# Optimization experiments

Measured on AMD Instinct MI355X. Metric: run time of the kernel, lower is better.

The kernel has to match this reference:

```python
import jax, jax.numpy as jnp
import numpy as np

N, C, R = 8192, 512, 8
DK = C // R  # 64

def setup_inputs() -> dict:
    key = jax.random.key(0)
    k1, k2, kq, kk, kv = jax.random.split(key, 5)
    s = 0.05
    return {
        "im1": jax.random.normal(k1, (N, C), jnp.float32),
        "im2": jax.random.normal(k2, (N, C), jnp.float32),
        "Wq": jax.random.normal(kq, (C, DK), jnp.float32) * s,
        "Wk": jax.random.normal(kk, (C, DK), jnp.float32) * s,
        "Wv": jax.random.normal(kv, (C, C), jnp.float32) * s,
    }

def reference(im1, im2, Wq, Wk, Wv):
    # shared projections (weights stored as [in, out]; torch Linear is x @ W.T)
    im1_q = im1 @ Wq  # [N, DK]
    im1_k = im1 @ Wk  # [N, DK]
    im1_v = im1 @ Wv  # [N, C]
    im2_q = im2 @ Wq
    im2_k = im2 @ Wk
    im2_v = im2 @ Wv
    # cross attention (no scaling in original)
    im1_attn = jax.nn.softmax(im2_q @ im1_k.T, axis=-1)  # [N, N]
    im2_attn = jax.nn.softmax(im1_q @ im2_k.T, axis=-1)  # [N, N]
    im1_out = im1_attn @ im1_v + im1
    im2_out = im2_attn @ im2_v + im2
    return im1_out, im2_out
```

## Files before the change

### kernel.cpp

```cpp
#include <hip/hip_runtime.h>

#define NN 8192
#define CC 512
#define DKK 64

typedef float f32x4 __attribute__((ext_vector_type(4)));
typedef float f32x16 __attribute__((ext_vector_type(16)));
typedef _Float16 f16x8 __attribute__((ext_vector_type(8)));
typedef _Float16 f16x4 __attribute__((ext_vector_type(4)));

__device__ __forceinline__ f32x4 mfma16(f16x8 a, f16x8 b, f32x4 c) {
    return __builtin_amdgcn_mfma_f32_16x16x32_f16(a, b, c, 0, 0, 0);
}
__device__ __forceinline__ f32x16 mfma32(f16x8 a, f16x8 b, f32x16 c) {
    return __builtin_amdgcn_mfma_f32_32x32x16_f16(a, b, c, 0, 0, 0);
}
__device__ __forceinline__ f16x8 scl8(f16x8 v, float f) {
    _Float16 h = (_Float16)f;
    f16x8 r;
#pragma unroll
    for (int i = 0; i < 8; i++) r[i] = v[i] * h;
    return r;
}

__global__ void wtrans_all_kernel(const float* __restrict__ Wq, const float* __restrict__ Wk,
                                  const float* __restrict__ Wv,
                                  _Float16* __restrict__ Wqt, _Float16* __restrict__ Wkt,
                                  _Float16* __restrict__ Wvf) {
    int idx = blockIdx.x * 256 + threadIdx.x;
    if (idx < 32768) {
        int n = idx >> 9, k = idx & 511;
        Wqt[idx] = (_Float16)Wq[k * 64 + n];
    } else if (idx < 65536) {
        int j = idx - 32768;
        int n = j >> 9, k = j & 511;
        Wkt[j] = (_Float16)Wk[k * 64 + n];
    } else {
        int j = idx - 65536;
        int k16 = j & 15, c = (j >> 4) & 511, ks = j >> 13;
        Wvf[j] = (_Float16)Wv[(size_t)(16 * ks + k16) * 512 + c];
    }
}

__global__ __launch_bounds__(256) void proj_qk2_kernel(
    const float* __restrict__ im1, const float* __restrict__ im2,
    const _Float16* __restrict__ Wqt, const _Float16* __restrict__ Wkt,
    _Float16* __restrict__ Q1, _Float16* __restrict__ Kf1,
    _Float16* __restrict__ Q2, _Float16* __restrict__ Kf2)
{
    const float* X = blockIdx.y ? im2 : im1;
    _Float16* Q = blockIdx.y ? Q2 : Q1;
    _Float16* Kf = blockIdx.y ? Kf2 : Kf1;

    __shared__ __align__(16) _Float16 Wlds[128 * 512];

    const int tid = threadIdx.x;
    const int lane = tid & 63, wave = tid >> 6;
    const int n16 = lane & 15, quad = lane >> 4;

#pragma unroll
    for (int i = 0; i < 32; i++) {
        const int idx = tid + 256 * i;
        const int row = idx >> 6, ch = idx & 63;
        const _Float16* src = (row < 64) ? (Wqt + (size_t)row * 512 + ch * 8)
                                         : (Wkt + (size_t)(row - 64) * 512 + ch * 8);
        *(f16x8*)&Wlds[row * 512 + ((ch ^ (row & 7)) * 8)] = *(const f16x8*)src;
    }
    __syncthreads();

    const int arow = blockIdx.x * 64 + wave * 16 + n16;
    f32x4 acc[8];
#pragma unroll
    for (int i = 0; i < 8; i++) acc[i] = (f32x4){0.f, 0.f, 0.f, 0.f};

    const float* xbase = X + (size_t)arow * 512 + quad * 8;
    for (int kk = 0; kk < 16; kk++) {
        f32x4 xa = *(const f32x4*)(xbase + kk * 32);
        f32x4 xb = *(const f32x4*)(xbase + kk * 32 + 4);
        f16x8 afrag;
#pragma unroll
        for (int j = 0; j < 4; j++) { afrag[j] = (_Float16)xa[j]; afrag[4 + j] = (_Float16)xb[j]; }
#pragma unroll
        for (int t = 0; t < 8; t++) {
            const int row = t * 16 + n16;
            f16x8 bfr = *(const f16x8*)&Wlds[row * 512 + (((4 * kk + quad) ^ (row & 7)) * 8)];
            acc[t] = mfma16(afrag, bfr, acc[t]);
        }
    }
    const int rbase = blockIdx.x * 64 + wave * 16 + quad * 4;
#pragma unroll
    for (int t = 0; t < 4; t++)
#pragma unroll
        for (int r = 0; r < 4; r++) {
            Q[(size_t)(rbase + r) * 64 + t * 16 + n16] = (_Float16)acc[t][r];
            Kf[((size_t)(blockIdx.x * 4 + t) * 64 + (wave * 16 + quad * 4 + r)) * 16 + n16] =
                (_Float16)acc[4 + t][r];
        }
}

__global__ __launch_bounds__(256) void proj_vt_kernel(
    const float* __restrict__ im1, const float* __restrict__ im2,
    const _Float16* __restrict__ Wvf,
    _Float16* __restrict__ Vf1, _Float16* __restrict__ Vf2)
{
    const float* X = blockIdx.y ? im2 : im1;
    _Float16* Vf = blockIdx.y ? Vf2 : Vf1;
    const int n0 = blockIdx.x * 32;
    const int tid = threadIdx.x;
    const int lane = tid & 63, wave = tid >> 6;
    const int l31 = lane & 31, lhi = lane >> 5;

    __shared__ __align__(16) _Float16 Xlds[32 * 512];

#pragma unroll
    for (int i = 0; i < 8; i++) {
        const int n = tid >> 3;
        const int chunk = (tid & 7) + 8 * i;
        const float* xp = X + (size_t)(n0 + n) * CC + chunk * 8;
        f32x4 x0 = *(const f32x4*)xp;
        f32x4 x1 = *(const f32x4*)(xp + 4);
        f16x8 d;
#pragma unroll
        for (int j = 0; j < 4; j++) { d[j] = (_Float16)x0[j]; d[4 + j] = (_Float16)x1[j]; }
        *(f16x8*)&Xlds[n * 512 + ((chunk ^ (n & 7)) * 8)] = d;
    }
    __syncthreads();

    f32x16 acc[4];
#pragma unroll
    for (int t = 0; t < 4; t++)
#pragma unroll
        for (int r = 0; r < 16; r++) acc[t][r] = 0.f;

    for (int ks = 0; ks < 32; ks++) {
        f16x8 xb = *(const f16x8*)&Xlds[l31 * 512 + (((2 * ks + lhi) ^ (l31 & 7)) * 8)];
#pragma unroll
        for (int ct = 0; ct < 4; ct++) {
            const _Float16* wp = Wvf + ((size_t)ks * 512 + 128 * wave + 32 * ct + l31) * 16 + 8 * lhi;
            acc[ct] = mfma32(*(const f16x8*)wp, xb, acc[ct]);
        }
    }
    const int tile = n0 >> 6;
    const int ksbase = (n0 & 32) >> 4;
#pragma unroll
    for (int ct = 0; ct < 4; ct++)
#pragma unroll
        for (int r = 0; r < 16; r++) {
            const int c = 128 * wave + 32 * ct + (r & 3) + 8 * (r >> 2) + 4 * lhi;
            const int ks = ksbase + (l31 >> 4);
            Vf[((size_t)(tile * 4 + ks) * 512 + c) * 16 + (l31 & 15)] = (_Float16)acc[ct][r];
        }
}

__global__ __launch_bounds__(512, 4) void flash6_kernel(
    const _Float16* __restrict__ Q1, const _Float16* __restrict__ Kf1,
    const _Float16* __restrict__ Q2, const _Float16* __restrict__ Kf2,
    const _Float16* __restrict__ Vf1, const _Float16* __restrict__ Vf2,
    const float* __restrict__ im1, const float* __restrict__ im2,
    float* __restrict__ out)
{
    const int img = blockIdx.y;
    const _Float16* Q = img ? Q1 : Q2;
    const _Float16* Kf = img ? Kf2 : Kf1;
    const _Float16* Vf = img ? Vf2 : Vf1;
    const float* res = img ? im2 : im1;
    float* o = out + (size_t)img * NN * CC;

    __shared__ __align__(16) _Float16 P[2][4][8][32][8];
    __shared__ float mPart[2][4][2][32];
    __shared__ float mF[4][2][32], lF[4][2][32];

    const int tid = threadIdx.x;
    const int lane = tid & 63, w = tid >> 6;
    const int l31 = lane & 31, lhi = lane >> 5;
    const int g = w >> 1, a = w & 1;
    const int qbase = blockIdx.x * 32;

    f16x8 qf[4];
    {
        const _Float16* qp = Q + (size_t)(qbase + l31) * DKK + 8 * lhi;
#pragma unroll
        for (int k = 0; k < 4; k++) qf[k] = *(const f16x8*)(qp + 16 * k);
    }

    f32x16 acc[2];
#pragma unroll
    for (int t = 0; t < 2; t++)
#pragma unroll
        for (int r = 0; r < 16; r++) acc[t][r] = 0.f;

    float ma_run = -3e38f, l_run = 0.f;
    float mg_run = -3e38f;

    const _Float16* kb = Kf + ((size_t)(32 * a + l31)) * 16 + 8 * lhi;
    const _Float16* vb = Vf + ((size_t)(64 * w + l31)) * 16 + 8 * lhi;

    auto do_qk = [&](int s) {
        const int t = 4 * s + g;
        const int pbuf = s & 1;
        f32x16 sA;
#pragma unroll
        for (int r = 0; r < 16; r++) sA[r] = 0.f;
#pragma unroll
        for (int k = 0; k < 4; k++) {
            f16x8 kf = *(const f16x8*)(kb + (size_t)(t * 4 + k) * (64 * 16));
            sA = mfma32(kf, qf[k], sA);
        }
        float mr[8];
#pragma unroll
        for (int i = 0; i < 8; i++) mr[i] = fmaxf(sA[i], sA[i + 8]);
#pragma unroll
        for (int i = 0; i < 4; i++) mr[i] = fmaxf(mr[i], mr[i + 4]);
        float mx = fmaxf(fmaxf(mr[0], mr[1]), fmaxf(mr[2], mr[3]));
        mx = fmaxf(mx, __shfl_xor(mx, 32));
        const float manew = fmaxf(ma_run, mx);
        if (lane < 32) mPart[pbuf][g][a][lane] = manew;
        float ls = 0.f;
#pragma unroll
        for (int r = 0; r < 16; r++) {
            float p = __expf(sA[r] - manew);
            ls += p;
            sA[r] = p;
        }
        ls += __shfl_xor(ls, 32);
        l_run = l_run * __expf(ma_run - manew) + ls;
        ma_run = manew;
#pragma unroll
        for (int gg = 0; gg < 4; gg++) {
            f16x4 p4;
#pragma unroll
            for (int u = 0; u < 4; u++) p4[u] = (_Float16)sA[gg * 4 + u];
            *(f16x4*)&P[pbuf][g][4 * a + gg][l31][4 * lhi] = p4;
        }
    };

    do_qk(0);
    __syncthreads();

    for (int s = 0; s < 32; s++) {
        const int pbuf = s & 1;

        f16x8 va0[8];
#pragma unroll
        for (int tt = 0; tt < 4; tt++)
#pragma unroll
            for (int ct = 0; ct < 2; ct++)
                va0[tt * 2 + ct] = *(const f16x8*)(vb +
                    ((size_t)((4 * s + tt) * 4) * 512 + 32 * ct) * 16);

        if (s < 31) do_qk(s + 1);

        float f[4][2];
        float mgn = mg_run;
#pragma unroll
        for (int g2 = 0; g2 < 4; g2++)
#pragma unroll
            for (int a2 = 0; a2 < 2; a2++) {
                f[g2][a2] = mPart[pbuf][g2][a2][l31];
                mgn = fmaxf(mgn, f[g2][a2]);
            }
        const float al = __expf(mg_run - mgn);
        mg_run = mgn;
        if (!__all(al == 1.f)) {
#pragma unroll
            for (int t = 0; t < 2; t++)
#pragma unroll
                for (int r = 0; r < 16; r++) acc[t][r] *= al;
        }
        bool nos1 = true;
#pragma unroll
        for (int g2 = 0; g2 < 4; g2++)
#pragma unroll
            for (int a2 = 0; a2 < 2; a2++) {
                f[g2][a2] = __expf(f[g2][a2] - mgn);
                nos1 &= (f[g2][a2] == 1.f);
            }
        const bool nos = __all(nos1);

#pragma unroll
        for (int tt = 0; tt < 4; tt++)
#pragma unroll
            for (int k = 0; k < 4; k++) {
                f16x8 pb = *(const f16x8*)&P[pbuf][tt][2 * k + lhi][l31][0];
                if (!nos) pb = scl8(pb, f[tt][k >> 1]);
#pragma unroll
                for (int ct = 0; ct < 2; ct++) {
                    f16x8 va = (k == 0) ? va0[tt * 2 + ct]
                        : *(const f16x8*)(vb +
                            ((size_t)((4 * s + tt) * 4 + k) * 512 + 32 * ct) * 16);
                    acc[ct] = mfma32(va, pb, acc[ct]);
                }
            }
        __syncthreads();
    }

    if (lane < 32) {
        mF[g][a][lane] = ma_run;
        lF[g][a][lane] = l_run;
    }
    __syncthreads();

    const float M = mg_run;
    float den = 0.f;
#pragma unroll
    for (int g2 = 0; g2 < 4; g2++)
#pragma unroll
        for (int a2 = 0; a2 < 2; a2++)
            den += lF[g2][a2][l31] * __expf(mF[g2][a2][l31] - M);
    const float fac = 1.f / den;

#pragma unroll
    for (int ct = 0; ct < 2; ct++)
#pragma unroll
        for (int rg = 0; rg < 4; rg++) {
            const int c = 64 * w + 32 * ct + 8 * rg + 4 * lhi;
            const size_t off = (size_t)(qbase + l31) * CC + c;
            f32x4 v;
#pragma unroll
            for (int u = 0; u < 4; u++) v[u] = acc[ct][4 * rg + u] * fac;
            f32x4 r4 = *(const f32x4*)(res + off);
            *(f32x4*)(o + off) = v + r4;
        }
}

extern "C" void kernel_launch(void* const* d_in, const int* in_sizes, int n_in,
                              void* d_out, int out_size, void* d_ws, size_t ws_size,
                              hipStream_t stream) {
    const float* im1 = (const float*)d_in[0];
    const float* im2 = (const float*)d_in[1];
    const float* Wq  = (const float*)d_in[2];
    const float* Wk  = (const float*)d_in[3];
    const float* Wv  = (const float*)d_in[4];
    float* out = (float*)d_out;

    _Float16* w = (_Float16*)d_ws;
    _Float16* Wqt = w;
    _Float16* Wkt = Wqt + 64 * 512;
    _Float16* Wvf = Wkt + 64 * 512;
    _Float16* Q1  = Wvf + 512 * 512;
    _Float16* Kf1 = Q1 + NN * DKK;
    _Float16* Q2  = Kf1 + NN * DKK;
    _Float16* Kf2 = Q2 + NN * DKK;
    _Float16* Vf1 = Kf2 + NN * DKK;
    _Float16* Vf2 = Vf1 + (size_t)CC * NN;

    wtrans_all_kernel<<<1280, 256, 0, stream>>>(Wq, Wk, Wv, Wqt, Wkt, Wvf);
    proj_qk2_kernel<<<dim3(128, 2), 256, 0, stream>>>(im1, im2, Wqt, Wkt, Q1, Kf1, Q2, Kf2);
    proj_vt_kernel<<<dim3(256, 2), 256, 0, stream>>>(im1, im2, Wvf, Vf1, Vf2);
    flash6_kernel<<<dim3(256, 2), 512, 0, stream>>>(Q1, Kf1, Q2, Kf2, Vf1, Vf2, im1, im2, out);
}
```

Measured before the change: 356.5 us.

## Process 64 queries per block so each V fragment feeds two query halves

The flash attention kernel now uses 1024-thread blocks that each cover 64 query rows instead of 32. Each wave owns 32 value channels across both 32-query halves, so every V fragment loaded from global memory is reused by two MFMAs. This halves V traffic per query. The grid becomes 256 blocks with the image index interleaved into blockIdx.x. In exchange, each block has larger shared-memory P and max buffers, per-half rescaling bookkeeping, a larger block synchronized by each barrier, and a launch-bounds setting that may tighten the register budget.

```diff
diff --git a/kernel.cpp b/kernel.cpp
--- a/kernel.cpp
+++ b/kernel.cpp
@@ -152,33 +152,34 @@
         }
 }
 
-__global__ __launch_bounds__(512, 4) void flash6_kernel(
+__global__ __launch_bounds__(1024, 4) void flash7_kernel(
     const _Float16* __restrict__ Q1, const _Float16* __restrict__ Kf1,
     const _Float16* __restrict__ Q2, const _Float16* __restrict__ Kf2,
     const _Float16* __restrict__ Vf1, const _Float16* __restrict__ Vf2,
     const float* __restrict__ im1, const float* __restrict__ im2,
     float* __restrict__ out)
 {
-    const int img = blockIdx.y;
+    const int bid = blockIdx.x;
+    const int img = bid & 1;
+    const int qbase = (bid >> 1) * 64;
     const _Float16* Q = img ? Q1 : Q2;
     const _Float16* Kf = img ? Kf2 : Kf1;
     const _Float16* Vf = img ? Vf2 : Vf1;
     const float* res = img ? im2 : im1;
     float* o = out + (size_t)img * NN * CC;
 
-    __shared__ __align__(16) _Float16 P[2][4][8][32][8];
-    __shared__ float mPart[2][4][2][32];
-    __shared__ float mF[4][2][32], lF[4][2][32];
+    __shared__ __align__(16) _Float16 P[2][4][8][64][8];
+    __shared__ float mPart[2][4][2][64];
+    __shared__ float mF[4][2][64], lF[4][2][64];
 
     const int tid = threadIdx.x;
     const int lane = tid & 63, w = tid >> 6;
     const int l31 = lane & 31, lhi = lane >> 5;
-    const int g = w >> 1, a = w & 1;
-    const int qbase = blockIdx.x * 32;
+    const int g = w >> 2, a = (w >> 1) & 1, b = w & 1;
 
     f16x8 qf[4];
     {
-        const _Float16* qp = Q + (size_t)(qbase + l31) * DKK + 8 * lhi;
+        const _Float16* qp = Q + (size_t)(qbase + 32 * b + l31) * DKK + 8 * lhi;
 #pragma unroll
         for (int k = 0; k < 4; k++) qf[k] = *(const f16x8*)(qp + 16 * k);
     }
@@ -190,10 +191,10 @@
         for (int r = 0; r < 16; r++) acc[t][r] = 0.f;
 
     float ma_run = -3e38f, l_run = 0.f;
-    float mg_run = -3e38f;
+    float mg_run[2] = {-3e38f, -3e38f};
 
     const _Float16* kb = Kf + ((size_t)(32 * a + l31)) * 16 + 8 * lhi;
-    const _Float16* vb = Vf + ((size_t)(64 * w + l31)) * 16 + 8 * lhi;
+    const _Float16* vb = Vf + ((size_t)(32 * w + l31)) * 16 + 8 * lhi;
 
     auto do_qk = [&](int s) {
         const int t = 4 * s + g;
@@ -214,7 +215,7 @@
         float mx = fmaxf(fmaxf(mr[0], mr[1]), fmaxf(mr[2], mr[3]));
         mx = fmaxf(mx, __shfl_xor(mx, 32));
         const float manew = fmaxf(ma_run, mx);
-        if (lane < 32) mPart[pbuf][g][a][lane] = manew;
+        if (lane < 32) mPart[pbuf][g][a][32 * b + lane] = manew;
         float ls = 0.f;
 #pragma unroll
         for (int r = 0; r < 16; r++) {
@@ -230,7 +231,7 @@
             f16x4 p4;
 #pragma unroll
             for (int u = 0; u < 4; u++) p4[u] = (_Float16)sA[gg * 4 + u];
-            *(f16x4*)&P[pbuf][g][4 * a + gg][l31][4 * lhi] = p4;
+            *(f16x4*)&P[pbuf][g][4 * a + gg][32 * b + l31][4 * lhi] = p4;
         }
     };
 
@@ -240,84 +241,91 @@
     for (int s = 0; s < 32; s++) {
         const int pbuf = s & 1;
 
-        f16x8 va0[8];
+        f16x8 va0[4];
 #pragma unroll
         for (int tt = 0; tt < 4; tt++)
-#pragma unroll
-            for (int ct = 0; ct < 2; ct++)
-                va0[tt * 2 + ct] = *(const f16x8*)(vb +
-                    ((size_t)((4 * s + tt) * 4) * 512 + 32 * ct) * 16);
+            va0[tt] = *(const f16x8*)(vb + ((size_t)((4 * s + tt) * 4) * 512) * 16);
 
         if (s < 31) do_qk(s + 1);
 
-        float f[4][2];
-        float mgn = mg_run;
-#pragma unroll
-        for (int g2 = 0; g2 < 4; g2++)
-#pragma unroll
-            for (int a2 = 0; a2 < 2; a2++) {
-                f[g2][a2] = mPart[pbuf][g2][a2][l31];
-                mgn = fmaxf(mgn, f[g2][a2]);
-            }
-        const float al = __expf(mg_run - mgn);
-        mg_run = mgn;
-        if (!__all(al == 1.f)) {
-#pragma unroll
-            for (int t = 0; t < 2; t++)
-#pragma unroll
-                for (int r = 0; r < 16; r++) acc[t][r] *= al;
-        }
+        float f[2][4][2];
         bool nos1 = true;
-#pragma unroll
-        for (int g2 = 0; g2 < 4; g2++)
-#pragma unroll
-            for (int a2 = 0; a2 < 2; a2++) {
-                f[g2][a2] = __expf(f[g2][a2] - mgn);
-                nos1 &= (f[g2][a2] == 1.f);
-            }
+        float al[2];
+#pragma unroll
+        for (int qh = 0; qh < 2; qh++) {
+            float mgn = mg_run[qh];
+#pragma unroll
+            for (int g2 = 0; g2 < 4; g2++)
+#pragma unroll
+                for (int a2 = 0; a2 < 2; a2++) {
+                    f[qh][g2][a2] = mPart[pbuf][g2][a2][32 * qh + l31];
+                    mgn = fmaxf(mgn, f[qh][g2][a2]);
+                }
+            al[qh] = __expf(mg_run[qh] - mgn);
+            mg_run[qh] = mgn;
+#pragma unroll
+            for (int g2 = 0; g2 < 4; g2++)
+#pragma unroll
+                for (int a2 = 0; a2 < 2; a2++) {
+                    f[qh][g2][a2] = __expf(f[qh][g2][a2] - mgn);
+                    nos1 &= (f[qh][g2][a2] == 1.f);
+                }
+        }
+        if (!__all((al[0] == 1.f) & (al[1] == 1.f))) {
+#pragma unroll
+            for (int qh = 0; qh < 2; qh++)
+#pragma unroll
+                for (int r = 0; r < 16; r++) acc[qh][r] *= al[qh];
+        }
         const bool nos = __all(nos1);
 
 #pragma unroll
         for (int tt = 0; tt < 4; tt++)
 #pragma unroll
             for (int k = 0; k < 4; k++) {
-                f16x8 pb = *(const f16x8*)&P[pbuf][tt][2 * k + lhi][l31][0];
-                if (!nos) pb = scl8(pb, f[tt][k >> 1]);
-#pragma unroll
-                for (int ct = 0; ct < 2; ct++) {
-                    f16x8 va = (k == 0) ? va0[tt * 2 + ct]
-                        : *(const f16x8*)(vb +
-                            ((size_t)((4 * s + tt) * 4 + k) * 512 + 32 * ct) * 16);
-                    acc[ct] = mfma32(va, pb, acc[ct]);
+                f16x8 pb0 = *(const f16x8*)&P[pbuf][tt][2 * k + lhi][l31][0];
+                f16x8 pb1 = *(const f16x8*)&P[pbuf][tt][2 * k + lhi][32 + l31][0];
+                if (!nos) {
+                    pb0 = scl8(pb0, f[0][tt][k >> 1]);
+                    pb1 = scl8(pb1, f[1][tt][k >> 1]);
                 }
+                f16x8 va = (k == 0) ? va0[tt]
+                    : *(const f16x8*)(vb + ((size_t)((4 * s + tt) * 4 + k) * 512) * 16);
+                acc[0] = mfma32(va, pb0, acc[0]);
+                acc[1] = mfma32(va, pb1, acc[1]);
             }
         __syncthreads();
     }
 
     if (lane < 32) {
-        mF[g][a][lane] = ma_run;
-        lF[g][a][lane] = l_run;
+        mF[g][a][32 * b + lane] = ma_run;
+        lF[g][a][32 * b + lane] = l_run;
     }
     __syncthreads();
 
-    const float M = mg_run;
-    float den = 0.f;
-#pragma unroll
-    for (int g2 = 0; g2 < 4; g2++)
-#pragma unroll
-        for (int a2 = 0; a2 < 2; a2++)
-            den += lF[g2][a2][l31] * __expf(mF[g2][a2][l31] - M);
-    const float fac = 1.f / den;
-
-#pragma unroll
-    for (int ct = 0; ct < 2; ct++)
+    float fac[2];
+#pragma unroll
+    for (int qh = 0; qh < 2; qh++) {
+        const int q = 32 * qh + l31;
+        const float M = mg_run[qh];
+        float den = 0.f;
+#pragma unroll
+        for (int g2 = 0; g2 < 4; g2++)
+#pragma unroll
+            for (int a2 = 0; a2 < 2; a2++)
+                den += lF[g2][a2][q] * __expf(mF[g2][a2][q] - M);
+        fac[qh] = 1.f / den;
+    }
+
+#pragma unroll
+    for (int qh = 0; qh < 2; qh++)
 #pragma unroll
         for (int rg = 0; rg < 4; rg++) {
-            const int c = 64 * w + 32 * ct + 8 * rg + 4 * lhi;
-            const size_t off = (size_t)(qbase + l31) * CC + c;
+            const int c = 32 * w + 8 * rg + 4 * lhi;
+            const size_t off = (size_t)(qbase + 32 * qh + l31) * CC + c;
             f32x4 v;
 #pragma unroll
-            for (int u = 0; u < 4; u++) v[u] = acc[ct][4 * rg + u] * fac;
+            for (int u = 0; u < 4; u++) v[u] = acc[qh][4 * rg + u] * fac[qh];
             f32x4 r4 = *(const f32x4*)(res + off);
             *(f32x4*)(o + off) = v + r4;
         }
@@ -347,5 +355,5 @@
     wtrans_all_kernel<<<1280, 256, 0, stream>>>(Wq, Wk, Wv, Wqt, Wkt, Wvf);
     proj_qk2_kernel<<<dim3(128, 2), 256, 0, stream>>>(im1, im2, Wqt, Wkt, Q1, Kf1, Q2, Kf2);
     proj_vt_kernel<<<dim3(256, 2), 256, 0, stream>>>(im1, im2, Wvf, Vf1, Vf2);
-    flash6_kernel<<<dim3(256, 2), 512, 0, stream>>>(Q1, Kf1, Q2, Kf2, Vf1, Vf2, im1, im2, out);
-}
+    flash7_kernel<<<256, 1024, 0, stream>>>(Q1, Kf1, Q2, Kf2, Vf1, Vf2, im1, im2, out);
+}
```

Result: no change. 363.1 us (+1.9%).

## Specialize flash waves into QK-softmax producers and PV consumers, use exp2

Applied to the files above, without the earlier changes.

Splits the eight waves of the attention kernel into two roles. Four waves compute QK scores and softmax for two key sub-tiles each, and four waves do the PV accumulation over 128 channels each. This lets the score computation of the next step overlap with the value accumulation of the current step. Q is prescaled by log2(e) during projection so softmax can use a hardware exp2. The split adds per-wave register pressure and an uneven MFMA load between roles, and it always rescales P.

```diff
diff --git a/kernel.cpp b/kernel.cpp
--- a/kernel.cpp
+++ b/kernel.cpp
@@ -15,13 +15,17 @@
 __device__ __forceinline__ f32x16 mfma32(f16x8 a, f16x8 b, f32x16 c) {
     return __builtin_amdgcn_mfma_f32_32x32x16_f16(a, b, c, 0, 0, 0);
 }
-__device__ __forceinline__ f16x8 scl8(f16x8 v, float f) {
-    _Float16 h = (_Float16)f;
+__device__ __forceinline__ f16x8 sclh8(f16x8 v, _Float16 h) {
     f16x8 r;
 #pragma unroll
     for (int i = 0; i < 8; i++) r[i] = v[i] * h;
     return r;
 }
+#if __has_builtin(__builtin_amdgcn_exp2f)
+__device__ __forceinline__ float exp2fast(float x) { return __builtin_amdgcn_exp2f(x); }
+#else
+__device__ __forceinline__ float exp2fast(float x) { return exp2f(x); }
+#endif
 
 __global__ void wtrans_all_kernel(const float* __restrict__ Wq, const float* __restrict__ Wk,
                                   const float* __restrict__ Wv,
@@ -92,7 +96,7 @@
     for (int t = 0; t < 4; t++)
 #pragma unroll
         for (int r = 0; r < 4; r++) {
-            Q[(size_t)(rbase + r) * 64 + t * 16 + n16] = (_Float16)acc[t][r];
+            Q[(size_t)(rbase + r) * 64 + t * 16 + n16] = (_Float16)(acc[t][r] * 1.44269504f);
             Kf[((size_t)(blockIdx.x * 4 + t) * 64 + (wave * 16 + quad * 4 + r)) * 16 + n16] =
                 (_Float16)acc[4 + t][r];
         }
@@ -152,7 +156,7 @@
         }
 }
 
-__global__ __launch_bounds__(512, 4) void flash6_kernel(
+__global__ __launch_bounds__(512, 4) void flash8_kernel(
     const _Float16* __restrict__ Q1, const _Float16* __restrict__ Kf1,
     const _Float16* __restrict__ Q2, const _Float16* __restrict__ Kf2,
     const _Float16* __restrict__ Vf1, const _Float16* __restrict__ Vf2,
@@ -165,6 +169,7 @@
     const _Float16* Vf = img ? Vf2 : Vf1;
     const float* res = img ? im2 : im1;
     float* o = out + (size_t)img * NN * CC;
+    const int qbase = blockIdx.x * 32;
 
     __shared__ __align__(16) _Float16 P[2][4][8][32][8];
     __shared__ float mPart[2][4][2][32];
@@ -173,154 +178,156 @@
     const int tid = threadIdx.x;
     const int lane = tid & 63, w = tid >> 6;
     const int l31 = lane & 31, lhi = lane >> 5;
-    const int g = w >> 1, a = w & 1;
-    const int qbase = blockIdx.x * 32;
+    const int role = (w ^ (w >> 2)) & 1;
+    const int gid = w >> 1;
 
     f16x8 qf[4];
-    {
+    float ma_run[2] = {-3e38f, -3e38f}, l_run[2] = {0.f, 0.f};
+    f32x16 acc[4];
+    float mg_run = -3e38f;
+
+    if (role == 0) {
         const _Float16* qp = Q + (size_t)(qbase + l31) * DKK + 8 * lhi;
 #pragma unroll
         for (int k = 0; k < 4; k++) qf[k] = *(const f16x8*)(qp + 16 * k);
-    }
-
-    f32x16 acc[2];
-#pragma unroll
-    for (int t = 0; t < 2; t++)
-#pragma unroll
-        for (int r = 0; r < 16; r++) acc[t][r] = 0.f;
-
-    float ma_run = -3e38f, l_run = 0.f;
-    float mg_run = -3e38f;
-
-    const _Float16* kb = Kf + ((size_t)(32 * a + l31)) * 16 + 8 * lhi;
-    const _Float16* vb = Vf + ((size_t)(64 * w + l31)) * 16 + 8 * lhi;
+    } else {
+#pragma unroll
+        for (int t = 0; t < 4; t++)
+#pragma unroll
+            for (int r = 0; r < 16; r++) acc[t][r] = 0.f;
+    }
+
+    const _Float16* kb = Kf + (size_t)l31 * 16 + 8 * lhi;
+    const _Float16* vb = Vf + (size_t)(128 * gid + l31) * 16 + 8 * lhi;
 
     auto do_qk = [&](int s) {
-        const int t = 4 * s + g;
+        const int t = 4 * s + gid;
         const int pbuf = s & 1;
-        f32x16 sA;
-#pragma unroll
-        for (int r = 0; r < 16; r++) sA[r] = 0.f;
-#pragma unroll
-        for (int k = 0; k < 4; k++) {
-            f16x8 kf = *(const f16x8*)(kb + (size_t)(t * 4 + k) * (64 * 16));
-            sA = mfma32(kf, qf[k], sA);
-        }
-        float mr[8];
-#pragma unroll
-        for (int i = 0; i < 8; i++) mr[i] = fmaxf(sA[i], sA[i + 8]);
-#pragma unroll
-        for (int i = 0; i < 4; i++) mr[i] = fmaxf(mr[i], mr[i + 4]);
-        float mx = fmaxf(fmaxf(mr[0], mr[1]), fmaxf(mr[2], mr[3]));
-        mx = fmaxf(mx, __shfl_xor(mx, 32));
-        const float manew = fmaxf(ma_run, mx);
-        if (lane < 32) mPart[pbuf][g][a][lane] = manew;
-        float ls = 0.f;
-#pragma unroll
-        for (int r = 0; r < 16; r++) {
-            float p = __expf(sA[r] - manew);
-            ls += p;
-            sA[r] = p;
-        }
-        ls += __shfl_xor(ls, 32);
-        l_run = l_run * __expf(ma_run - manew) + ls;
-        ma_run = manew;
-#pragma unroll
-        for (int gg = 0; gg < 4; gg++) {
-            f16x4 p4;
-#pragma unroll
-            for (int u = 0; u < 4; u++) p4[u] = (_Float16)sA[gg * 4 + u];
-            *(f16x4*)&P[pbuf][g][4 * a + gg][l31][4 * lhi] = p4;
+#pragma unroll
+        for (int a2 = 0; a2 < 2; a2++) {
+            f32x16 sA;
+#pragma unroll
+            for (int r = 0; r < 16; r++) sA[r] = 0.f;
+#pragma unroll
+            for (int k = 0; k < 4; k++) {
+                f16x8 kf = *(const f16x8*)(kb + (size_t)((t * 4 + k) * 64 + 32 * a2) * 16);
+                sA = mfma32(kf, qf[k], sA);
+            }
+            float mr[8];
+#pragma unroll
+            for (int i = 0; i < 8; i++) mr[i] = fmaxf(sA[i], sA[i + 8]);
+#pragma unroll
+            for (int i = 0; i < 4; i++) mr[i] = fmaxf(mr[i], mr[i + 4]);
+            float mx = fmaxf(fmaxf(mr[0], mr[1]), fmaxf(mr[2], mr[3]));
+            mx = fmaxf(mx, __shfl_xor(mx, 32));
+            const float manew = fmaxf(ma_run[a2], mx);
+            if (lane < 32) mPart[pbuf][gid][a2][lane] = manew;
+            float ls = 0.f;
+#pragma unroll
+            for (int r = 0; r < 16; r++) {
+                float p = exp2fast(sA[r] - manew);
+                ls += p;
+                sA[r] = p;
+            }
+            ls += __shfl_xor(ls, 32);
+            l_run[a2] = l_run[a2] * exp2fast(ma_run[a2] - manew) + ls;
+            ma_run[a2] = manew;
+#pragma unroll
+            for (int gg = 0; gg < 4; gg++) {
+                f16x4 p4;
+#pragma unroll
+                for (int u = 0; u < 4; u++) p4[u] = (_Float16)sA[gg * 4 + u];
+                *(f16x4*)&P[pbuf][gid][4 * a2 + gg][l31][4 * lhi] = p4;
+            }
         }
     };
 
-    do_qk(0);
+    if (role == 0) do_qk(0);
     __syncthreads();
 
     for (int s = 0; s < 32; s++) {
         const int pbuf = s & 1;
-
-        f16x8 va0[8];
-#pragma unroll
-        for (int tt = 0; tt < 4; tt++)
-#pragma unroll
-            for (int ct = 0; ct < 2; ct++)
-                va0[tt * 2 + ct] = *(const f16x8*)(vb +
-                    ((size_t)((4 * s + tt) * 4) * 512 + 32 * ct) * 16);
-
-        if (s < 31) do_qk(s + 1);
-
-        float f[4][2];
-        float mgn = mg_run;
+        if (role == 0) {
+            if (s < 31) do_qk(s + 1);
+        } else {
+            f16x8 va_pre[4];
+#pragma unroll
+            for (int ct = 0; ct < 4; ct++)
+                va_pre[ct] = *(const f16x8*)(vb + (size_t)((4 * s) * 4 * 512 + 32 * ct * 512 / 512 * 512) * 0 +
+                                             (size_t)((4 * s) * 4 * 512 + 32 * ct) * 16);
+            float m[4][2];
+            float mgn = mg_run;
+#pragma unroll
+            for (int g2 = 0; g2 < 4; g2++)
+#pragma unroll
+                for (int a2 = 0; a2 < 2; a2++) {
+                    m[g2][a2] = mPart[pbuf][g2][a2][l31];
+                    mgn = fmaxf(mgn, m[g2][a2]);
+                }
+            const float al = exp2fast(mg_run - mgn);
+            mg_run = mgn;
+            _Float16 fh[4][2];
+#pragma unroll
+            for (int g2 = 0; g2 < 4; g2++)
+#pragma unroll
+                for (int a2 = 0; a2 < 2; a2++)
+                    fh[g2][a2] = (_Float16)exp2fast(m[g2][a2] - mgn);
+            if (!__all(al == 1.f)) {
+#pragma unroll
+                for (int t = 0; t < 4; t++)
+#pragma unroll
+                    for (int r = 0; r < 16; r++) acc[t][r] *= al;
+            }
+#pragma unroll
+            for (int tt = 0; tt < 4; tt++) {
+                const int t = 4 * s + tt;
+#pragma unroll
+                for (int k = 0; k < 4; k++) {
+                    f16x8 pb = *(const f16x8*)&P[pbuf][tt][2 * k + lhi][l31][0];
+                    pb = sclh8(pb, fh[tt][k >> 1]);
+#pragma unroll
+                    for (int ct = 0; ct < 4; ct++) {
+                        f16x8 va = (tt == 0 && k == 0) ? va_pre[ct]
+                            : *(const f16x8*)(vb + (size_t)((t * 4 + k) * 512 + 32 * ct) * 16);
+                        acc[ct] = mfma32(va, pb, acc[ct]);
+                    }
+                }
+            }
+        }
+        __syncthreads();
+    }
+
+    if (role == 0 && lane < 32) {
+#pragma unroll
+        for (int a2 = 0; a2 < 2; a2++) {
+            mF[gid][a2][lane] = ma_run[a2];
+            lF[gid][a2][lane] = l_run[a2];
+        }
+    }
+    __syncthreads();
+
+    if (role == 1) {
+        const float M = mg_run;
+        float den = 0.f;
 #pragma unroll
         for (int g2 = 0; g2 < 4; g2++)
 #pragma unroll
-            for (int a2 = 0; a2 < 2; a2++) {
-                f[g2][a2] = mPart[pbuf][g2][a2][l31];
-                mgn = fmaxf(mgn, f[g2][a2]);
-            }
-        const float al = __expf(mg_run - mgn);
-        mg_run = mgn;
-        if (!__all(al == 1.f)) {
-#pragma unroll
-            for (int t = 0; t < 2; t++)
-#pragma unroll
-                for (int r = 0; r < 16; r++) acc[t][r] *= al;
-        }
-        bool nos1 = true;
-#pragma unroll
-        for (int g2 = 0; g2 < 4; g2++)
-#pragma unroll
-            for (int a2 = 0; a2 < 2; a2++) {
-                f[g2][a2] = __expf(f[g2][a2] - mgn);
-                nos1 &= (f[g2][a2] == 1.f);
-            }
-        const bool nos = __all(nos1);
-
-#pragma unroll
-        for (int tt = 0; tt < 4; tt++)
-#pragma unroll
-            for (int k = 0; k < 4; k++) {
-                f16x8 pb = *(const f16x8*)&P[pbuf][tt][2 * k + lhi][l31][0];
-                if (!nos) pb = scl8(pb, f[tt][k >> 1]);
-#pragma unroll
-                for (int ct = 0; ct < 2; ct++) {
-                    f16x8 va = (k == 0) ? va0[tt * 2 + ct]
-                        : *(const f16x8*)(vb +
-                            ((size_t)((4 * s + tt) * 4 + k) * 512 + 32 * ct) * 16);
-                    acc[ct] = mfma32(va, pb, acc[ct]);
-                }
-            }
-        __syncthreads();
-    }
-
-    if (lane < 32) {
-        mF[g][a][lane] = ma_run;
-        lF[g][a][lane] = l_run;
-    }
-    __syncthreads();
-
-    const float M = mg_run;
-    float den = 0.f;
-#pragma unroll
-    for (int g2 = 0; g2 < 4; g2++)
-#pragma unroll
-        for (int a2 = 0; a2 < 2; a2++)
-            den += lF[g2][a2][l31] * __expf(mF[g2][a2][l31] - M);
-    const float fac = 1.f / den;
-
-#pragma unroll
-    for (int ct = 0; ct < 2; ct++)
-#pragma unroll
-        for (int rg = 0; rg < 4; rg++) {
-            const int c = 64 * w + 32 * ct + 8 * rg + 4 * lhi;
-            const size_t off = (size_t)(qbase + l31) * CC + c;
-            f32x4 v;
-#pragma unroll
-            for (int u = 0; u < 4; u++) v[u] = acc[ct][4 * rg + u] * fac;
-            f32x4 r4 = *(const f32x4*)(res + off);
-            *(f32x4*)(o + off) = v + r4;
-        }
+            for (int a2 = 0; a2 < 2; a2++)
+                den += lF[g2][a2][l31] * exp2fast(mF[g2][a2][l31] - M);
+        const float fac = 1.f / den;
+#pragma unroll
+        for (int ct = 0; ct < 4; ct++)
+#pragma unroll
+            for (int rg = 0; rg < 4; rg++) {
+                const int c = 128 * gid + 32 * ct + 8 * rg + 4 * lhi;
+                const size_t off = (size_t)(qbase + l31) * CC + c;
+                f32x4 v;
+#pragma unroll
+                for (int u = 0; u < 4; u++) v[u] = acc[ct][4 * rg + u] * fac;
+                f32x4 r4 = *(const f32x4*)(res + off);
+                *(f32x4*)(o + off) = v + r4;
+            }
+    }
 }
 
 extern "C" void kernel_launch(void* const* d_in, const int* in_sizes, int n_in,
@@ -347,5 +354,5 @@
     wtrans_all_kernel<<<1280, 256, 0, stream>>>(Wq, Wk, Wv, Wqt, Wkt, Wvf);
     proj_qk2_kernel<<<dim3(128, 2), 256, 0, stream>>>(im1, im2, Wqt, Wkt, Q1, Kf1, Q2, Kf2);
     proj_vt_kernel<<<dim3(256, 2), 256, 0, stream>>>(im1, im2, Wvf, Vf1, Vf2);
-    flash6_kernel<<<dim3(256, 2), 512, 0, stream>>>(Q1, Kf1, Q2, Kf2, Vf1, Vf2, im1, im2, out);
-}
+    flash8_kernel<<<dim3(256, 2), 512, 0, stream>>>(Q1, Kf1, Q2, Kf2, Vf1, Vf2, im1, im2, out);
+}
```

Result: slower. 756.6 us (+112.2%).
